# Kernel tuning notes

Hardware: AMD Instinct MI355X
Metric: run time of the kernel (lower is better)

The kernel has to match this reference:

```python
import jax, jax.numpy as jnp
import numpy as np

B, H, LQ, LK, DK = 4, 8, 256, 256, 64

def setup_inputs() -> dict:
    key = jax.random.key(0)
    ks = jax.random.split(key, 9)
    s = 1.0 / np.sqrt(DK)
    return {
        "q": jax.random.normal(ks[0], (B, H, LQ, DK), jnp.float32),
        "k": jax.random.normal(ks[1], (B, H, LK, DK), jnp.float32),
        "v": jax.random.normal(ks[2], (B, H, LK, DK), jnp.float32),
        "Wq_w": jax.random.uniform(ks[3], (DK, DK), jnp.float32, -s, s),
        "Wq_b": jax.random.uniform(ks[4], (DK,), jnp.float32, -s, s),
        "Wk_w": jax.random.uniform(ks[5], (DK, DK), jnp.float32, -s, s),
        "Wk_b": jax.random.uniform(ks[6], (DK,), jnp.float32, -s, s),
        "vs_w": jax.random.uniform(ks[7], (1, DK), jnp.float32, -s, s),
        "vs_b": jax.random.uniform(ks[8], (1,), jnp.float32, -s, s),
    }

def reference(q, k, v, Wq_w, Wq_b, Wk_w, Wk_b, vs_w, vs_b):
    # Additive (Bahdanau) attention; dropout is identity at eval time.
    qp = jnp.einsum('bhqd,ed->bhqe', q, Wq_w) + Wq_b          # [B,H,Lq,d_k]
    kp = jnp.einsum('bhkd,ed->bhke', k, Wk_w) + Wk_b          # [B,H,Lk,d_k]
    # Broadcast add -> tanh -> linear projection to scalar score
    feat = jnp.tanh(qp[:, :, :, None, :] + kp[:, :, None, :, :])  # [B,H,Lq,Lk,d_k]
    scores = jnp.einsum('bhqkd,d->bhqk', feat, vs_w[0]) + vs_b[0]  # [B,H,Lq,Lk]
    attn = jax.nn.softmax(scores, axis=-1)
    output = jnp.einsum('bhqk,bhkd->bhqd', attn, v)
    return output, attn
```

## Files before the change

### kernel.cpp

```cpp
#include <hip/hip_runtime.h>

#define B_ 4
#define H_ 8
#define LQ_ 256
#define LK_ 256
#define DK_ 64
#define BH_ (B_*H_)
#define NROWS (BH_*LQ_)
#define QT 4

__global__ __launch_bounds__(256) void proj_kernel(
    const float* __restrict__ qin, const float* __restrict__ kin,
    const float* __restrict__ Wq, const float* __restrict__ bq,
    const float* __restrict__ Wk, const float* __restrict__ bk,
    float* __restrict__ qp, float* __restrict__ kp)
{
    const int which = blockIdx.x >> 8;
    const int rb    = (blockIdx.x & 255) * 32;
    const float* in   = which ? kin : qin;
    const float* W    = which ? Wk  : Wq;
    const float* bias = which ? bk  : bq;
    float* out        = which ? kp  : qp;

    __shared__ float in_s[32*68];
    __shared__ float w_s[64*68];
    const int tid = threadIdx.x;

    {
        const float4* g = (const float4*)(in + rb*64);
        #pragma unroll
        for (int p = 0; p < 2; ++p) {
            int f = tid + p*256;
            float4 x = g[f];
            *(float4*)&in_s[(f>>4)*68 + (f&15)*4] = x;
        }
    }
    {
        const float4* g = (const float4*)W;
        #pragma unroll
        for (int p = 0; p < 4; ++p) {
            int f = tid + p*256;
            float4 x = g[f];
            *(float4*)&w_s[(f>>4)*68 + (f&15)*4] = x;
        }
    }
    __syncthreads();

    const int r  = tid >> 3;
    const int gg = tid & 7;
    float acc[8];
    #pragma unroll
    for (int i = 0; i < 8; ++i) acc[i] = 0.f;

    #pragma unroll
    for (int j = 0; j < 16; ++j) {
        float4 x = *(const float4*)&in_s[r*68 + j*4];
        #pragma unroll
        for (int i = 0; i < 8; ++i) {
            const int e = gg + i*8;
            float4 w = *(const float4*)&w_s[e*68 + j*4];
            acc[i] = fmaf(w.x, x.x, acc[i]);
            acc[i] = fmaf(w.y, x.y, acc[i]);
            acc[i] = fmaf(w.z, x.z, acc[i]);
            acc[i] = fmaf(w.w, x.w, acc[i]);
        }
    }
    float* orow = out + (rb + r)*64;
    #pragma unroll
    for (int i = 0; i < 8; ++i) {
        const int e = gg + i*8;
        orow[e] = acc[i] + bias[e];
    }
}

__global__ __launch_bounds__(256) void score_softmax_kernel(
    const float* __restrict__ qp, const float* __restrict__ kp,
    const float* __restrict__ vs_w, const float* __restrict__ vs_b,
    float* __restrict__ attn)
{
    const int bh = blockIdx.x >> 6;
    const int qt = blockIdx.x & 63;
    const int t  = threadIdx.x;
    const int lane = t & 63, wid = t >> 6;

    const float C2  = 2.8853900817779268f;
    const float L2E = 1.4426950408889634f;

    __shared__ float qp_s[QT*64];
    __shared__ float vs_s[64];
    __shared__ float reds[QT][4];

    if (t < QT*16) {
        float4 x = ((const float4*)(qp + (bh*LQ_ + qt*QT)*64))[t];
        x.x *= C2; x.y *= C2; x.z *= C2; x.w *= C2;
        ((float4*)qp_s)[t] = x;
    } else if (t < QT*16 + 64) {
        vs_s[t - QT*16] = vs_w[t - QT*16];
    }
    __syncthreads();

    float S = vs_b[0];
    #pragma unroll
    for (int j = 0; j < 16; ++j) {
        float4 w = *(const float4*)&vs_s[j*4];
        S += (w.x + w.y) + (w.z + w.w);
    }

    const float4* kg = (const float4*)(kp + (bh*LK_ + t)*64);

    float sc[QT] = {0.f, 0.f, 0.f, 0.f};
    #pragma unroll 1
    for (int quar = 0; quar < 4; ++quar) {
        float4 kr[4];
        #pragma unroll
        for (int j = 0; j < 4; ++j) {
            float4 kv = kg[quar*4 + j];
            kr[j].x = kv.x*C2; kr[j].y = kv.y*C2;
            kr[j].z = kv.z*C2; kr[j].w = kv.w*C2;
        }
        #pragma unroll
        for (int q = 0; q < QT; ++q) {
            float a0 = 0.f, a1 = 0.f;
            #pragma unroll
            for (int j = 0; j < 4; ++j) {
                float4 qv = *(const float4*)&qp_s[q*64 + quar*16 + j*4];
                float4 wv = *(const float4*)&vs_s[quar*16 + j*4];
                float4 kv = kr[j];
                a0 = fmaf(wv.x, __builtin_amdgcn_rcpf(__builtin_amdgcn_exp2f(qv.x+kv.x)+1.f), a0);
                a1 = fmaf(wv.y, __builtin_amdgcn_rcpf(__builtin_amdgcn_exp2f(qv.y+kv.y)+1.f), a1);
                a0 = fmaf(wv.z, __builtin_amdgcn_rcpf(__builtin_amdgcn_exp2f(qv.z+kv.z)+1.f), a0);
                a1 = fmaf(wv.w, __builtin_amdgcn_rcpf(__builtin_amdgcn_exp2f(qv.w+kv.w)+1.f), a1);
            }
            sc[q] += a0 + a1;
        }
    }

    float p[QT];
    #pragma unroll
    for (int q = 0; q < QT; ++q) {
        p[q] = __builtin_amdgcn_exp2f((S - 2.f*sc[q]) * L2E);
        float s = p[q];
        #pragma unroll
        for (int off = 32; off; off >>= 1) s += __shfl_xor(s, off, 64);
        if (lane == 0) reds[q][wid] = s;
    }
    __syncthreads();
    #pragma unroll
    for (int q = 0; q < QT; ++q) {
        float s = (reds[q][0] + reds[q][1]) + (reds[q][2] + reds[q][3]);
        float a = p[q] * __builtin_amdgcn_rcpf(s);
        attn[(bh*LQ_ + qt*QT + q)*LK_ + t] = a;
    }
}

__global__ __launch_bounds__(256) void pv_kernel(
    const float* __restrict__ attn, const float* __restrict__ v,
    float* __restrict__ out)
{
    const int bh = blockIdx.x >> 4;
    const int q0 = (blockIdx.x & 15) * 16;
    const int t  = threadIdx.x;
    const int dg = t & 15;
    const int rg = t >> 4;

    __shared__ float at_s[16*68];
    __shared__ float v_s[64*64];

    float4 acc = {0.f, 0.f, 0.f, 0.f};
    for (int c = 0; c < 4; ++c) {
        {
            int row = t >> 4, k0 = (t & 15) * 4;
            float4 a4 = *(const float4*)&attn[(bh*LQ_ + q0 + row)*LK_ + c*64 + k0];
            *(float4*)&at_s[row*68 + k0] = a4;
        }
        #pragma unroll
        for (int p = 0; p < 4; ++p) {
            int f = t + p*256;
            int kk = f >> 4, col = (f & 15) * 4;
            *(float4*)&v_s[kk*64 + col] =
                *(const float4*)&v[(bh*LK_ + c*64 + kk)*DK_ + col];
        }
        __syncthreads();
        #pragma unroll
        for (int kkg = 0; kkg < 16; ++kkg) {
            float av[4];
            *(float4*)av = *(const float4*)&at_s[rg*68 + kkg*4];
            #pragma unroll
            for (int u = 0; u < 4; ++u) {
                float4 vv = *(const float4*)&v_s[(kkg*4+u)*64 + dg*4];
                acc.x = fmaf(av[u], vv.x, acc.x);
                acc.y = fmaf(av[u], vv.y, acc.y);
                acc.z = fmaf(av[u], vv.z, acc.z);
                acc.w = fmaf(av[u], vv.w, acc.w);
            }
        }
        __syncthreads();
    }
    *(float4*)&out[(bh*LQ_ + q0 + rg)*DK_ + dg*4] = acc;
}

extern "C" void kernel_launch(void* const* d_in, const int* in_sizes, int n_in,
                              void* d_out, int out_size, void* d_ws, size_t ws_size,
                              hipStream_t stream) {
    const float* q    = (const float*)d_in[0];
    const float* k    = (const float*)d_in[1];
    const float* v    = (const float*)d_in[2];
    const float* Wq_w = (const float*)d_in[3];
    const float* Wq_b = (const float*)d_in[4];
    const float* Wk_w = (const float*)d_in[5];
    const float* Wk_b = (const float*)d_in[6];
    const float* vs_w = (const float*)d_in[7];
    const float* vs_b = (const float*)d_in[8];

    float* out  = (float*)d_out;
    float* attn = out + B_*H_*LQ_*DK_;
    float* qp   = (float*)d_ws;
    float* kp   = qp + NROWS*64;

    proj_kernel<<<512, 256, 0, stream>>>(q, k, Wq_w, Wq_b, Wk_w, Wk_b, qp, kp);
    score_softmax_kernel<<<BH_*(LQ_/QT), 256, 0, stream>>>(qp, kp, vs_w, vs_b, attn);
    pv_kernel<<<BH_*(LQ_/16), 256, 0, stream>>>(attn, v, out);
}
```

Baseline: 122.4 us.

## Fuse attention-times-V into score/softmax kernel using shared-memory attn rows

Removes the separate PV kernel. The score/softmax kernel now keeps its QT attention rows in shared memory and computes output = attn·V directly, with one thread per (query, d) pair reading V from global memory. This saves a kernel launch and the re-read of the attn matrix from global memory. In exchange, V for each bh is re-read by 64 blocks instead of 16, with no shared-memory tiling, and each thread runs a serial 256-long dot product.

```diff
diff --git a/kernel.cpp b/kernel.cpp
--- a/kernel.cpp
+++ b/kernel.cpp
@@ -57,8 +57,7 @@
         float4 x = *(const float4*)&in_s[r*68 + j*4];
         #pragma unroll
         for (int i = 0; i < 8; ++i) {
-            const int e = gg + i*8;
-            float4 w = *(const float4*)&w_s[e*68 + j*4];
+            float4 w = *(const float4*)&w_s[(gg + i*8)*68 + j*4];
             acc[i] = fmaf(w.x, x.x, acc[i]);
             acc[i] = fmaf(w.y, x.y, acc[i]);
             acc[i] = fmaf(w.z, x.z, acc[i]);
@@ -73,10 +72,11 @@
     }
 }
 
-__global__ __launch_bounds__(256) void score_softmax_kernel(
+__global__ __launch_bounds__(256) void score_softmax_pv_kernel(
     const float* __restrict__ qp, const float* __restrict__ kp,
     const float* __restrict__ vs_w, const float* __restrict__ vs_b,
-    float* __restrict__ attn)
+    const float* __restrict__ v,
+    float* __restrict__ attn, float* __restrict__ out)
 {
     const int bh = blockIdx.x >> 6;
     const int qt = blockIdx.x & 63;
@@ -89,6 +89,7 @@
     __shared__ float qp_s[QT*64];
     __shared__ float vs_s[64];
     __shared__ float reds[QT][4];
+    __shared__ float a_s[QT*256];
 
     if (t < QT*16) {
         float4 x = ((const float4*)(qp + (bh*LQ_ + qt*QT)*64))[t];
@@ -150,53 +151,24 @@
         float s = (reds[q][0] + reds[q][1]) + (reds[q][2] + reds[q][3]);
         float a = p[q] * __builtin_amdgcn_rcpf(s);
         attn[(bh*LQ_ + qt*QT + q)*LK_ + t] = a;
+        a_s[q*256 + t] = a;
     }
-}
+    __syncthreads();
 
-__global__ __launch_bounds__(256) void pv_kernel(
-    const float* __restrict__ attn, const float* __restrict__ v,
-    float* __restrict__ out)
-{
-    const int bh = blockIdx.x >> 4;
-    const int q0 = (blockIdx.x & 15) * 16;
-    const int t  = threadIdx.x;
-    const int dg = t & 15;
-    const int rg = t >> 4;
-
-    __shared__ float at_s[16*68];
-    __shared__ float v_s[64*64];
-
-    float4 acc = {0.f, 0.f, 0.f, 0.f};
-    for (int c = 0; c < 4; ++c) {
-        {
-            int row = t >> 4, k0 = (t & 15) * 4;
-            float4 a4 = *(const float4*)&attn[(bh*LQ_ + q0 + row)*LK_ + c*64 + k0];
-            *(float4*)&at_s[row*68 + k0] = a4;
+    {
+        const int q = t >> 6, d = t & 63;
+        const float* vb = v + bh*LK_*DK_ + d;
+        float acc = 0.f;
+        #pragma unroll 4
+        for (int k4 = 0; k4 < 64; ++k4) {
+            float4 a4 = *(const float4*)&a_s[q*256 + k4*4];
+            acc = fmaf(a4.x, vb[(k4*4+0)*64], acc);
+            acc = fmaf(a4.y, vb[(k4*4+1)*64], acc);
+            acc = fmaf(a4.z, vb[(k4*4+2)*64], acc);
+            acc = fmaf(a4.w, vb[(k4*4+3)*64], acc);
         }
-        #pragma unroll
-        for (int p = 0; p < 4; ++p) {
-            int f = t + p*256;
-            int kk = f >> 4, col = (f & 15) * 4;
-            *(float4*)&v_s[kk*64 + col] =
-                *(const float4*)&v[(bh*LK_ + c*64 + kk)*DK_ + col];
-        }
-        __syncthreads();
-        #pragma unroll
-        for (int kkg = 0; kkg < 16; ++kkg) {
-            float av[4];
-            *(float4*)av = *(const float4*)&at_s[rg*68 + kkg*4];
-            #pragma unroll
-            for (int u = 0; u < 4; ++u) {
-                float4 vv = *(const float4*)&v_s[(kkg*4+u)*64 + dg*4];
-                acc.x = fmaf(av[u], vv.x, acc.x);
-                acc.y = fmaf(av[u], vv.y, acc.y);
-                acc.z = fmaf(av[u], vv.z, acc.z);
-                acc.w = fmaf(av[u], vv.w, acc.w);
-            }
-        }
-        __syncthreads();
+        out[(bh*LQ_ + qt*QT + q)*DK_ + d] = acc;
     }
-    *(float4*)&out[(bh*LQ_ + q0 + rg)*DK_ + dg*4] = acc;
 }
 
 extern "C" void kernel_launch(void* const* d_in, const int* in_sizes, int n_in,
@@ -218,6 +190,6 @@
     float* kp   = qp + NROWS*64;
 
     proj_kernel<<<512, 256, 0, stream>>>(q, k, Wq_w, Wq_b, Wk_w, Wk_b, qp, kp);
-    score_softmax_kernel<<<BH_*(LQ_/QT), 256, 0, stream>>>(qp, kp, vs_w, vs_b, attn);
-    pv_kernel<<<BH_*(LQ_/16), 256, 0, stream>>>(attn, v, out);
+    score_softmax_pv_kernel<<<BH_*(LQ_/QT), 256, 0, stream>>>(
+        qp, kp, vs_w, vs_b, v, attn, out);
 }
```

Result: slower. 126.3 us (+3.2%).
